# Kernel optimization log

Hardware: AMD Instinct MI355X
Metric: run time of the kernel (lower is better)

The kernel has to match this reference:

```python
import jax, jax.numpy as jnp
import numpy as np

B, T, S, D = 8, 512, 512, 1024
NUM_HEADS = 16
REUSE_HEADS = 8
NEW_HEADS = NUM_HEADS - REUSE_HEADS
KEY_DIM = 64
VALUE_DIM = 64
PE_MAX = 512  # pe_max_seq_length


def setup_inputs() -> dict:
    key = jax.random.key(0)
    ks = jax.random.split(key, 12)
    s = 0.02
    return {
        "query": jax.random.normal(ks[0], (B, T, D), jnp.float32),
        "value": jax.random.normal(ks[1], (B, S, D), jnp.float32),
        # scores reused from a previous layer (already softmaxed there)
        "reuse_attention_scores": jax.random.uniform(ks[2], (B, REUSE_HEADS, T, S), jnp.float32),
        "Wq": jax.random.normal(ks[3], (D, NEW_HEADS, KEY_DIM), jnp.float32) * s,
        "bq": jnp.zeros((NEW_HEADS, KEY_DIM), jnp.float32),
        "Wk": jax.random.normal(ks[4], (D, NEW_HEADS, KEY_DIM), jnp.float32) * s,
        "bk": jnp.zeros((NEW_HEADS, KEY_DIM), jnp.float32),
        "Wv": jax.random.normal(ks[5], (D, NUM_HEADS, VALUE_DIM), jnp.float32) * s,
        "bv": jnp.zeros((NUM_HEADS, VALUE_DIM), jnp.float32),
        # relative position embeddings: [1, new_heads, 2*PE_MAX - 1]
        "pos_emb": jax.random.truncated_normal(ks[6], -2.0, 2.0, (1, NEW_HEADS, 2 * PE_MAX - 1), jnp.float32) * 0.2,
        # output denses: one for reused heads (no bias), one for new heads (bias)
        "Wo_reuse": jax.random.normal(ks[7], (REUSE_HEADS, VALUE_DIM, D), jnp.float32) * s,
        "Wo_new": jax.random.normal(ks[8], (NEW_HEADS, VALUE_DIM, D), jnp.float32) * s,
        "bo": jnp.zeros((D,), jnp.float32),
    }


def reference(query, value, reuse_attention_scores, Wq, bq, Wk, bk, Wv, bv,
              pos_emb, Wo_reuse, Wo_new, bo):
    # projections (EinsumDense abc,cde->abde + bias over last two dims)
    q = jnp.einsum("btd,dnh->btnh", query, Wq) + bq           # [B,T,Hn,kd]
    k = jnp.einsum("bsd,dnh->bsnh", value, Wk) + bk           # [B,S,Hn,kd]
    v = jnp.einsum("bsd,dnh->bsnh", value, Wv) + bv           # [B,S,H,vd]
    v_reuse, v_new = v[:, :, :REUSE_HEADS, :], v[:, :, REUSE_HEADS:, :]

    # new-head scores: scaled QK^T  (dot_product_equation 'aecd,abcd->acbe')
    q = q * (1.0 / np.sqrt(float(KEY_DIM)))
    new_scores = jnp.einsum("bsnh,btnh->bnts", k, q)          # [B,Hn,T,S]

    # relative position bias: index = clip(key_pos - query_pos + PE_MAX-1)
    rel = jnp.arange(S)[None, :] - jnp.arange(T)[:, None] + (PE_MAX - 1)
    rel = jnp.clip(rel, 0, 2 * PE_MAX - 2)                    # [T,S]
    bias = pos_emb[0][:, rel]                                 # [Hn,T,S]
    new_scores = jax.nn.softmax(new_scores + bias[None], axis=-1)

    # reused heads consume previous-layer scores directly (dropout=0)
    reuse_scores = reuse_attention_scores[:, :REUSE_HEADS]
    out_reuse = jnp.einsum("bnts,bsnh->btnh", reuse_scores, v_reuse)
    out_new = jnp.einsum("bnts,bsnh->btnh", new_scores, v_new)

    # separate output projections, summed; bias only on the new-heads dense
    out = (jnp.einsum("btnh,nhd->btd", out_reuse, Wo_reuse)
           + jnp.einsum("btnh,nhd->btd", out_new, Wo_new) + bo)
    return out
```

## Files before the change

kernel.cpp:

```cpp
#include <hip/hip_runtime.h>
#include <hip/hip_bf16.h>

typedef __bf16 bf16_t;
typedef __bf16 bf16x8 __attribute__((ext_vector_type(8)));
typedef float  f32x4  __attribute__((ext_vector_type(4)));

#define GLDS(gsrc, ldst)                                                              \
  __builtin_amdgcn_global_load_lds(                                                   \
      (const __attribute__((address_space(1))) unsigned int*)(gsrc),                  \
      (__attribute__((address_space(3))) unsigned int*)(ldst), 16, 0, 0)

struct TArgs {
  const float* src[5];
  bf16_t* dst[5];
  int C[5], Ct[5], off[5], blk0[6];
  float scale[5];
};
struct CTArgs {
  const float* qa; bf16_t* qd;
  const float* va; bf16_t* vd;
  TArgs ta;
};
__global__ void k_convtrans(CTArgs ca) {
  __shared__ float tile[32][33];
  const int bid = blockIdx.x;
  if (bid < 4096) {
    int i = bid * 256 + threadIdx.x;
    const float* s; bf16_t* d;
    if (i < 524288) { s = ca.qa; d = ca.qd; } else { s = ca.va; d = ca.vd; i -= 524288; }
    const float4* p = reinterpret_cast<const float4*>(s) + 2 * (long)i;
    float4 x = p[0], y = p[1];
    bf16x8 o;
    o[0] = (bf16_t)x.x; o[1] = (bf16_t)x.y; o[2] = (bf16_t)x.z; o[3] = (bf16_t)x.w;
    o[4] = (bf16_t)y.x; o[5] = (bf16_t)y.y; o[6] = (bf16_t)y.z; o[7] = (bf16_t)y.w;
    reinterpret_cast<bf16x8*>(d)[i] = o;
    return;
  }
  const TArgs& ta = ca.ta;
  const int tb = bid - 4096;
  int s = 0;
  while (tb >= ta.blk0[s + 1]) ++s;
  const int bi = tb - ta.blk0[s];
  const int Ct = ta.Ct[s];
  const int c0 = (bi % Ct) * 32, r0 = (bi / Ct) * 32;
  const int C = ta.C[s];
  const float* src = ta.src[s];
  const int lx = threadIdx.x & 31, ly = threadIdx.x >> 5;
  #pragma unroll
  for (int i = 0; i < 32; i += 8)
    tile[ly + i][lx] = src[(long)(r0 + ly + i) * C + (c0 + lx)];
  __syncthreads();
  const float sc = ta.scale[s];
  bf16_t* dst = ta.dst[s];
  const int off = ta.off[s];
  #pragma unroll
  for (int i = 0; i < 32; i += 8)
    dst[(long)(c0 + ly + i) * 1024 + off + (r0 + lx)] = (bf16_t)(tile[lx][ly + i] * sc);
}

struct ProjItem {
  const bf16_t* A; const bf16_t* B; bf16_t* C; const float* bias;
  float bscale; int ldc; int writeT;
};
struct ProjArgs { ProjItem it[3]; };

__global__ __launch_bounds__(256)
void k_gemm_proj(ProjArgs pa) {
  __shared__ char smem[32768];
  const int bid = blockIdx.x;
  const int z = bid < 128 ? 0 : (bid < 256 ? 1 : 2);
  const int local = bid - (z == 0 ? 0 : (z == 1 ? 128 : 256));
  const ProjItem it = pa.it[z];
  const int t = threadIdx.x, lane = t & 63, wid = t >> 6;
  const int wr = wid >> 1, wc = wid & 1;
  const int m0 = (local & 31) * 128, n0 = (local >> 5) * 128;
  const int lhi = lane >> 4, llo = lane & 15;

  const bf16_t* Ab = it.A + (long)m0 * 1024;
  const bf16_t* Bb = it.B + (long)n0 * 1024;

  const int e0 = t * 8,        r0s = e0 >> 5, c0s = e0 & 31;
  const int e1 = (256 + t) * 8, r1s = e1 >> 5, c1s = e1 & 31;

#define PSTAGE(k0_, bsel)                                                     \
  { bf16_t* bA = (bf16_t*)(smem + (bsel) * 16384);                            \
    bf16_t* bB = (bf16_t*)(smem + (bsel) * 16384 + 8192);                     \
    GLDS(Ab + (long)r0s * 1024 + (k0_) + c0s, bA + wid * 512);                \
    GLDS(Ab + (long)r1s * 1024 + (k0_) + c1s, bA + 2048 + wid * 512);         \
    GLDS(Bb + (long)r0s * 1024 + (k0_) + c0s, bB + wid * 512);                \
    GLDS(Bb + (long)r1s * 1024 + (k0_) + c1s, bB + 2048 + wid * 512); }

  f32x4 acc[4][4] = {};
  PSTAGE(0, 0);
  __syncthreads();
  int cur = 0;
  for (int t32 = 0; t32 < 32; ++t32) {
    bf16_t* sA = (bf16_t*)(smem + cur * 16384);
    bf16_t* sB = (bf16_t*)(smem + cur * 16384 + 8192);
    bf16x8 a[4], b[4];
    #pragma unroll
    for (int mi = 0; mi < 4; ++mi)
      a[mi] = *reinterpret_cast<const bf16x8*>(sA + (wr * 64 + mi * 16 + llo) * 32 + lhi * 8);
    #pragma unroll
    for (int ni = 0; ni < 4; ++ni)
      b[ni] = *reinterpret_cast<const bf16x8*>(sB + (wc * 64 + ni * 16 + llo) * 32 + lhi * 8);
    if (t32 < 31) PSTAGE((t32 + 1) * 32, cur ^ 1);
    #pragma unroll
    for (int mi = 0; mi < 4; ++mi)
      #pragma unroll
      for (int ni = 0; ni < 4; ++ni)
        acc[mi][ni] = __builtin_amdgcn_mfma_f32_16x16x32_bf16(a[mi], b[ni], acc[mi][ni], 0, 0, 0);
    __syncthreads();
    cur ^= 1;
  }
#undef PSTAGE

  #pragma unroll
  for (int mi = 0; mi < 4; ++mi)
    #pragma unroll
    for (int ni = 0; ni < 4; ++ni) {
      const float bv = it.bias[n0 + wc * 64 + ni * 16 + llo] * it.bscale;
      #pragma unroll
      for (int r = 0; r < 4; ++r) acc[mi][ni][r] += bv;
    }

  if (!it.writeT) {
    bf16_t* E = (bf16_t*)smem;
    #pragma unroll
    for (int p = 0; p < 2; ++p) {
      if (wr == p) {
        #pragma unroll
        for (int mi = 0; mi < 4; ++mi)
          #pragma unroll
          for (int ni = 0; ni < 4; ++ni)
            #pragma unroll
            for (int r = 0; r < 4; ++r)
              E[(mi * 16 + lhi * 4 + r) * 136 + wc * 64 + ni * 16 + llo] = (bf16_t)acc[mi][ni][r];
      }
      __syncthreads();
      #pragma unroll
      for (int round = 0; round < 4; ++round) {
        const int row = (t >> 4) + round * 16;
        const int l16 = t & 15;
        float4 v = *reinterpret_cast<const float4*>((char*)E + row * 272 + l16 * 16);
        *reinterpret_cast<float4*>(it.C + (long)(m0 + p * 64 + row) * it.ldc + n0 + l16 * 8) = v;
      }
      __syncthreads();
    }
  } else {
    bf16_t* E = (bf16_t*)smem;
    #pragma unroll
    for (int p = 0; p < 2; ++p) {
      if (wr == p) {
        #pragma unroll
        for (int mi = 0; mi < 4; ++mi)
          #pragma unroll
          for (int ni = 0; ni < 4; ++ni)
            #pragma unroll
            for (int r = 0; r < 4; ++r)
              E[(wc * 64 + ni * 16 + llo) * 72 + mi * 16 + lhi * 4 + r] = (bf16_t)acc[mi][ni][r];
      }
      __syncthreads();
      #pragma unroll
      for (int round = 0; round < 4; ++round) {
        const int nr = (t >> 3) + round * 32;
        const int l8 = t & 7;
        float4 v = *reinterpret_cast<const float4*>((char*)E + nr * 144 + l8 * 16);
        *reinterpret_cast<float4*>(it.C + (long)(n0 + nr) * it.ldc + m0 + p * 64 + l8 * 8) = v;
      }
      __syncthreads();
    }
  }
}

__global__ __launch_bounds__(256)
void k_gemm_out(const bf16_t* __restrict__ A_, const bf16_t* __restrict__ B_,
                float* __restrict__ C_, const float* __restrict__ bias) {
  __shared__ char smem[24576];
  const int t = threadIdx.x, lane = t & 63, wid = t >> 6;
  const int wr = wid >> 1, wc = wid & 1;
  const int m0 = blockIdx.x * 64, n0 = blockIdx.y * 128;
  const int lhi = lane >> 4, llo = lane & 15;

  const bf16_t* Ab = A_ + (long)m0 * 1024;
  const bf16_t* Bb = B_ + (long)n0 * 1024;

  const int e0 = t * 8,        r0s = e0 >> 5, c0s = e0 & 31;
  const int e1 = (256 + t) * 8, r1s = e1 >> 5, c1s = e1 & 31;

#define OSTAGE(k0_, bsel)                                                     \
  { bf16_t* bA = (bf16_t*)(smem + (bsel) * 12288);                            \
    bf16_t* bB = (bf16_t*)(smem + (bsel) * 12288 + 4096);                     \
    GLDS(Ab + (long)r0s * 1024 + (k0_) + c0s, bA + wid * 512);                \
    GLDS(Bb + (long)r0s * 1024 + (k0_) + c0s, bB + wid * 512);                \
    GLDS(Bb + (long)r1s * 1024 + (k0_) + c1s, bB + 2048 + wid * 512); }

  f32x4 acc[2][4] = {};
  OSTAGE(0, 0);
  __syncthreads();
  int cur = 0;
  for (int t32 = 0; t32 < 32; ++t32) {
    bf16_t* sA = (bf16_t*)(smem + cur * 12288);
    bf16_t* sB = (bf16_t*)(smem + cur * 12288 + 4096);
    bf16x8 a[2], b[4];
    #pragma unroll
    for (int mi = 0; mi < 2; ++mi)
      a[mi] = *reinterpret_cast<const bf16x8*>(sA + (wr * 32 + mi * 16 + llo) * 32 + lhi * 8);
    #pragma unroll
    for (int ni = 0; ni < 4; ++ni)
      b[ni] = *reinterpret_cast<const bf16x8*>(sB + (wc * 64 + ni * 16 + llo) * 32 + lhi * 8);
    if (t32 < 31) OSTAGE((t32 + 1) * 32, cur ^ 1);
    #pragma unroll
    for (int mi = 0; mi < 2; ++mi)
      #pragma unroll
      for (int ni = 0; ni < 4; ++ni)
        acc[mi][ni] = __builtin_amdgcn_mfma_f32_16x16x32_bf16(a[mi], b[ni], acc[mi][ni], 0, 0, 0);
    __syncthreads();
    cur ^= 1;
  }
#undef OSTAGE

  #pragma unroll
  for (int mi = 0; mi < 2; ++mi)
    #pragma unroll
    for (int ni = 0; ni < 4; ++ni) {
      const float bv = bias[n0 + wc * 64 + ni * 16 + llo];
      #pragma unroll
      for (int r = 0; r < 4; ++r) acc[mi][ni][r] += bv;
    }

  float* E = (float*)smem;
  #pragma unroll
  for (int p = 0; p < 2; ++p) {
    if (wr == p) {
      #pragma unroll
      for (int mi = 0; mi < 2; ++mi)
        #pragma unroll
        for (int ni = 0; ni < 4; ++ni)
          #pragma unroll
          for (int r = 0; r < 4; ++r)
            E[(mi * 16 + lhi * 4 + r) * 132 + wc * 64 + ni * 16 + llo] = acc[mi][ni][r];
    }
    __syncthreads();
    #pragma unroll
    for (int round = 0; round < 4; ++round) {
      const int row = (t >> 5) + round * 8;
      const int l32 = t & 31;
      float4 v = *reinterpret_cast<const float4*>((char*)E + row * 528 + l32 * 16);
      *reinterpret_cast<float4*>(C_ + (long)(m0 + p * 32 + row) * 1024 + n0 + l32 * 4) = v;
    }
    __syncthreads();
  }
}

__global__ __launch_bounds__(256, 5)
void k_attn_all(const bf16_t* __restrict__ qb, const bf16_t* __restrict__ kb,
                const bf16_t* __restrict__ vbT, const float* __restrict__ pe,
                const float* __restrict__ reuse, bf16_t* __restrict__ om) {
  __shared__ char smem[28672];
  const int bid = blockIdx.x;
  const int r3 = bid % 3;
  const int q3 = bid / 3;
  const int lane = threadIdx.x & 63, w = threadIdx.x >> 6;
  const int lhi = lane >> 4, llo = lane & 15;

  if (r3 == 0) {
    float* pes = (float*)smem;
    char* KtB = smem + 4096;
    char* VtB = smem + 12288;
    char* PtB = smem + 20480 + w * 2048;

    const int fidx = q3;
    const int tt = fidx >> 6;
    const int bh = fidx & 63;
    const int b = bh >> 3, h = bh & 7;
    const int t0w = tt * 64 + w * 16;

    const bf16_t* Ksrc = kb + (long)(b * 512) * 512 + h * 64;
    const bf16_t* Vsrc = vbT + (long)(512 + h * 64) * 4096 + b * 512;
    const int krow = w * 16 + (lane >> 3);
    const int kcol = ((lane & 7) ^ (lane >> 3)) << 3;
    bf16_t* kdst = (bf16_t*)(KtB + w * 2048);
    bf16_t* vdst = (bf16_t*)(VtB + w * 2048);

#define STAGE_K(it_)                                                                   \
  { _Pragma("unroll")                                                                  \
    for (int g = 0; g < 2; ++g)                                                        \
      GLDS(Ksrc + (long)((it_) * 64 + krow + g * 8) * 512 + kcol, kdst + g * 512); }
#define STAGE_V(it_)                                                                   \
  { _Pragma("unroll")                                                                  \
    for (int g = 0; g < 2; ++g)                                                        \
      GLDS(Vsrc + (long)(krow + g * 8) * 4096 + (it_) * 64 + kcol, vdst + g * 512); }

    STAGE_K(0);
    STAGE_V(0);

    const bf16_t* Qb = qb + (long)(b * 512 + t0w + llo) * 512 + h * 64;
    bf16x8 qf0 = *reinterpret_cast<const bf16x8*>(Qb + lhi * 8);
    bf16x8 qf1 = *reinterpret_cast<const bf16x8*>(Qb + 32 + lhi * 8);
    for (int i = threadIdx.x; i < 1023; i += 256) pes[i] = pe[h * 1023 + i];

    f32x4 oacc[4] = {};
    float lr[4] = {0.f, 0.f, 0.f, 0.f};

    __syncthreads();

    for (int it = 0; it < 8; ++it) {
      const int s0 = it * 64;

      f32x4 acc[4] = {};
      #pragma unroll
      for (int st = 0; st < 4; ++st) {
        const int rowb = st * 16 + llo;
        const int sw = (rowb & 7) << 4;
        bf16x8 kf0 = *reinterpret_cast<const bf16x8*>(KtB + rowb * 128 + ((lhi * 16) ^ sw));
        bf16x8 kf1 = *reinterpret_cast<const bf16x8*>(KtB + rowb * 128 + ((64 + lhi * 16) ^ sw));
        acc[st] = __builtin_amdgcn_mfma_f32_16x16x32_bf16(qf0, kf0, acc[st], 0, 0, 0);
        acc[st] = __builtin_amdgcn_mfma_f32_16x16x32_bf16(qf1, kf1, acc[st], 0, 0, 0);
      }

      __syncthreads();
      if (it < 7) STAGE_K(it + 1);

      #pragma unroll
      for (int r = 0; r < 4; ++r) {
        const int tl = lhi * 4 + r;
        const int bidx = s0 + llo - (t0w + tl) + 511;
        const int swp = (tl & 7) << 4;
        float lp = 0.f;
        #pragma unroll
        for (int st = 0; st < 4; ++st) {
          const float e = __expf(acc[st][r] + pes[bidx + st * 16]);
          lp += e;
          *reinterpret_cast<bf16_t*>(PtB + tl * 128 + (((st * 16 + llo) * 2) ^ swp)) = (bf16_t)e;
        }
        lr[r] += lp;
      }

      const int swa = (llo & 7) << 4;
      #pragma unroll
      for (int ks = 0; ks < 2; ++ks) {
        bf16x8 pav = *reinterpret_cast<const bf16x8*>(PtB + llo * 128 + ((ks * 64 + lhi * 16) ^ swa));
        #pragma unroll
        for (int ni = 0; ni < 4; ++ni) {
          const int rowv = ni * 16 + llo;
          bf16x8 vf = *reinterpret_cast<const bf16x8*>(VtB + rowv * 128 + ((ks * 64 + lhi * 16) ^ ((rowv & 7) << 4)));
          oacc[ni] = __builtin_amdgcn_mfma_f32_16x16x32_bf16(pav, vf, oacc[ni], 0, 0, 0);
        }
      }

      __syncthreads();
      if (it < 7) STAGE_V(it + 1);
    }

    #pragma unroll
    for (int r = 0; r < 4; ++r) {
      lr[r] += __shfl_xor(lr[r], 1);
      lr[r] += __shfl_xor(lr[r], 2);
      lr[r] += __shfl_xor(lr[r], 4);
      lr[r] += __shfl_xor(lr[r], 8);
    }

    bf16_t* Ew = (bf16_t*)(smem + 4096 + w * 4096);
    #pragma unroll
    for (int ni = 0; ni < 4; ++ni)
      #pragma unroll
      for (int r = 0; r < 4; ++r)
        Ew[(lhi * 4 + r) * 72 + ni * 16 + llo] = (bf16_t)(oacc[ni][r] * (1.f / lr[r]));
    #pragma unroll
    for (int round = 0; round < 2; ++round) {
      const int lr8 = (lane >> 3) + round * 8;
      const int l8 = lane & 7;
      float4 v = *reinterpret_cast<const float4*>((char*)Ew + lr8 * 144 + l8 * 16);
      *reinterpret_cast<float4*>(om + (long)(b * 512 + t0w + lr8) * 1024 + 512 + h * 64 + l8 * 8) = v;
    }
#undef STAGE_K
#undef STAGE_V
    return;
  }

  typedef float RedRow[32][68];
  RedRow* red = (RedRow*)smem;
  const int pidx = q3 * 2 + (r3 - 1);
  const int bh = pidx & 63;
  const int mt = pidx >> 6;
  const int b = bh >> 3, head = bh & 7;
  const int m0 = mt * 32;
  const int ks0 = w * 128;

  const float*  Af = reuse + (long)b * 2097152 + (long)head * 262144;
  const bf16_t* Bp = vbT + (long)(head * 64) * 4096 + b * 512;

  f32x4 acc[2][4] = {};
  float4 Ax[2][2][2];
  bf16x8 Bx[2][4];

  #define PV_LOAD(kq, buf)                                                              \
    {                                                                                   \
      const int kk = ks0 + (kq) * 32 + lhi * 8;                                         \
      _Pragma("unroll")                                                                 \
      for (int mi = 0; mi < 2; ++mi) {                                                  \
        const float4* p = reinterpret_cast<const float4*>(Af + (long)(m0 + mi * 16 + llo) * 512 + kk); \
        Ax[buf][mi][0] = p[0];                                                          \
        Ax[buf][mi][1] = p[1];                                                          \
      }                                                                                 \
      _Pragma("unroll")                                                                 \
      for (int ni = 0; ni < 4; ++ni)                                                    \
        Bx[buf][ni] = *reinterpret_cast<const bf16x8*>(Bp + (long)(ni * 16 + llo) * 4096 + kk); \
    }

  PV_LOAD(0, 0);
  #pragma unroll
  for (int kq = 0; kq < 4; ++kq) {
    const int cb = kq & 1;
    if (kq < 3) {
      const int nb = (kq + 1) & 1;
      PV_LOAD(kq + 1, nb);
    }
    bf16x8 a[2];
    #pragma unroll
    for (int mi = 0; mi < 2; ++mi) {
      float4 x = Ax[cb][mi][0], y = Ax[cb][mi][1];
      bf16x8 tv;
      tv[0] = (bf16_t)x.x; tv[1] = (bf16_t)x.y; tv[2] = (bf16_t)x.z; tv[3] = (bf16_t)x.w;
      tv[4] = (bf16_t)y.x; tv[5] = (bf16_t)y.y; tv[6] = (bf16_t)y.z; tv[7] = (bf16_t)y.w;
      a[mi] = tv;
    }
    #pragma unroll
    for (int mi = 0; mi < 2; ++mi)
      #pragma unroll
      for (int ni = 0; ni < 4; ++ni)
        acc[mi][ni] = __builtin_amdgcn_mfma_f32_16x16x32_bf16(a[mi], Bx[cb][ni], acc[mi][ni], 0, 0, 0);
  }
  #undef PV_LOAD

  if (w >= 2) {
    #pragma unroll
    for (int mi = 0; mi < 2; ++mi)
      #pragma unroll
      for (int ni = 0; ni < 4; ++ni)
        #pragma unroll
        for (int r = 0; r < 4; ++r)
          red[w - 2][mi * 16 + lhi * 4 + r][ni * 16 + llo] = acc[mi][ni][r];
  }
  __syncthreads();
  if (w < 2) {
    #pragma unroll
    for (int mi = 0; mi < 2; ++mi)
      #pragma unroll
      for (int ni = 0; ni < 4; ++ni)
        #pragma unroll
        for (int r = 0; r < 4; ++r)
          acc[mi][ni][r] += red[w][mi * 16 + lhi * 4 + r][ni * 16 + llo];
  }
  __syncthreads();
  if (w == 1) {
    #pragma unroll
    for (int mi = 0; mi < 2; ++mi)
      #pragma unroll
      for (int ni = 0; ni < 4; ++ni)
        #pragma unroll
        for (int r = 0; r < 4; ++r)
          red[0][mi * 16 + lhi * 4 + r][ni * 16 + llo] = acc[mi][ni][r];
  }
  __syncthreads();
  if (w == 0) {
    bf16_t* E = (bf16_t*)&red[1][0][0];
    #pragma unroll
    for (int mi = 0; mi < 2; ++mi)
      #pragma unroll
      for (int ni = 0; ni < 4; ++ni)
        #pragma unroll
        for (int r = 0; r < 4; ++r) {
          const int mr = mi * 16 + lhi * 4 + r;
          const int nn = ni * 16 + llo;
          E[mr * 72 + nn] = (bf16_t)(acc[mi][ni][r] + red[0][mr][nn]);
        }
    bf16_t* Cb = om + (long)b * 524288 + head * 64;
    #pragma unroll
    for (int round = 0; round < 4; ++round) {
      const int row = (lane >> 3) + round * 8;
      const int l8 = lane & 7;
      float4 v = *reinterpret_cast<const float4*>((char*)E + row * 144 + l8 * 16);
      *reinterpret_cast<float4*>(Cb + (long)(m0 + row) * 1024 + l8 * 8) = v;
    }
  }
}

extern "C" void kernel_launch(void* const* d_in, const int* in_sizes, int n_in,
                              void* d_out, int out_size, void* d_ws, size_t ws_size,
                              hipStream_t stream) {
  const float* query = (const float*)d_in[0];
  const float* value = (const float*)d_in[1];
  const float* reuse = (const float*)d_in[2];
  const float* Wq    = (const float*)d_in[3];
  const float* bq    = (const float*)d_in[4];
  const float* Wk    = (const float*)d_in[5];
  const float* bk    = (const float*)d_in[6];
  const float* Wv    = (const float*)d_in[7];
  const float* bv    = (const float*)d_in[8];
  const float* pe    = (const float*)d_in[9];
  const float* WoR   = (const float*)d_in[10];
  const float* WoN   = (const float*)d_in[11];
  const float* bo    = (const float*)d_in[12];
  float* out = (float*)d_out;
  (void)in_sizes; (void)n_in; (void)out_size; (void)ws_size;

  char* w = (char*)d_ws;
  bf16_t* qx  = (bf16_t*)(w);
  bf16_t* vx  = (bf16_t*)(w + (8L  << 20));
  bf16_t* WqT = (bf16_t*)(w + (16L << 20));
  bf16_t* WkT = (bf16_t*)(w + (17L << 20));
  bf16_t* WvT = (bf16_t*)(w + (18L << 20));
  bf16_t* WoT = (bf16_t*)(w + (20L << 20));
  bf16_t* qb  = (bf16_t*)(w + (22L << 20));
  bf16_t* kb  = (bf16_t*)(w + (26L << 20));
  bf16_t* vbT = (bf16_t*)(w + (30L << 20));
  bf16_t* om  = (bf16_t*)(w + (38L << 20));

  CTArgs ca;
  ca.qa = query; ca.qd = qx; ca.va = value; ca.vd = vx;
  ca.ta.src[0] = Wq;  ca.ta.dst[0] = WqT; ca.ta.C[0] = 512;  ca.ta.Ct[0] = 16; ca.ta.off[0] = 0;   ca.ta.scale[0] = 0.125f;
  ca.ta.src[1] = Wk;  ca.ta.dst[1] = WkT; ca.ta.C[1] = 512;  ca.ta.Ct[1] = 16; ca.ta.off[1] = 0;   ca.ta.scale[1] = 1.f;
  ca.ta.src[2] = Wv;  ca.ta.dst[2] = WvT; ca.ta.C[2] = 1024; ca.ta.Ct[2] = 32; ca.ta.off[2] = 0;   ca.ta.scale[2] = 1.f;
  ca.ta.src[3] = WoR; ca.ta.dst[3] = WoT; ca.ta.C[3] = 1024; ca.ta.Ct[3] = 32; ca.ta.off[3] = 0;   ca.ta.scale[3] = 1.f;
  ca.ta.src[4] = WoN; ca.ta.dst[4] = WoT; ca.ta.C[4] = 1024; ca.ta.Ct[4] = 32; ca.ta.off[4] = 512; ca.ta.scale[4] = 1.f;
  ca.ta.blk0[0] = 0; ca.ta.blk0[1] = 512; ca.ta.blk0[2] = 1024; ca.ta.blk0[3] = 2048; ca.ta.blk0[4] = 2560; ca.ta.blk0[5] = 3072;
  k_convtrans<<<dim3(7168), 256, 0, stream>>>(ca);

  ProjArgs pa;
  pa.it[0] = { qx, WqT, qb,  bq, 0.125f, 512,  0 };
  pa.it[1] = { vx, WkT, kb,  bk, 1.f,    512,  0 };
  pa.it[2] = { vx, WvT, vbT, bv, 1.f,    4096, 1 };
  k_gemm_proj<<<dim3(512), 256, 0, stream>>>(pa);

  k_attn_all<<<dim3(1536), 256, 0, stream>>>(qb, kb, vbT, pe, reuse, om);

  k_gemm_out<<<dim3(64, 8), 256, 0, stream>>>(om, WoT, out, bo);
}
```

Baseline: 89.28 us.

## Double-buffer K/V tiles in LDS and deepen A prefetch in reuse path

In the new-head attention path, K and V tiles are now staged into two LDS buffers. The next iteration's tiles are issued at the top of each loop iteration, which removes one of the two per-iteration barriers. In the reuse-score path, loads of the fp32 score matrix are prefetched two steps ahead with a triple buffer, while V loads stay double-buffered. The cost is more LDS (45 KB vs 28 KB) and more registers, so launch bounds drop from 5 to 3 blocks per CU, which reduces occupancy.

```diff
diff --git a/kernel.cpp b/kernel.cpp
--- a/kernel.cpp
+++ b/kernel.cpp
@@ -253,11 +253,11 @@
   }
 }
 
-__global__ __launch_bounds__(256, 5)
+__global__ __launch_bounds__(256, 3)
 void k_attn_all(const bf16_t* __restrict__ qb, const bf16_t* __restrict__ kb,
                 const bf16_t* __restrict__ vbT, const float* __restrict__ pe,
                 const float* __restrict__ reuse, bf16_t* __restrict__ om) {
-  __shared__ char smem[28672];
+  __shared__ char smem[45056];
   const int bid = blockIdx.x;
   const int r3 = bid % 3;
   const int q3 = bid / 3;
@@ -266,9 +266,7 @@
 
   if (r3 == 0) {
     float* pes = (float*)smem;
-    char* KtB = smem + 4096;
-    char* VtB = smem + 12288;
-    char* PtB = smem + 20480 + w * 2048;
+    char* PtB = smem + 36864 + w * 2048;
 
     const int fidx = q3;
     const int tt = fidx >> 6;
@@ -280,20 +278,17 @@
     const bf16_t* Vsrc = vbT + (long)(512 + h * 64) * 4096 + b * 512;
     const int krow = w * 16 + (lane >> 3);
     const int kcol = ((lane & 7) ^ (lane >> 3)) << 3;
-    bf16_t* kdst = (bf16_t*)(KtB + w * 2048);
-    bf16_t* vdst = (bf16_t*)(VtB + w * 2048);
-
-#define STAGE_K(it_)                                                                   \
-  { _Pragma("unroll")                                                                  \
-    for (int g = 0; g < 2; ++g)                                                        \
-      GLDS(Ksrc + (long)((it_) * 64 + krow + g * 8) * 512 + kcol, kdst + g * 512); }
-#define STAGE_V(it_)                                                                   \
-  { _Pragma("unroll")                                                                  \
-    for (int g = 0; g < 2; ++g)                                                        \
-      GLDS(Vsrc + (long)(krow + g * 8) * 4096 + (it_) * 64 + kcol, vdst + g * 512); }
-
-    STAGE_K(0);
-    STAGE_V(0);
+
+#define STAGE_KV(it_, b_)                                                              \
+  { bf16_t* kdst = (bf16_t*)(smem + 4096 + (b_) * 8192 + w * 2048);                    \
+    bf16_t* vdst = (bf16_t*)(smem + 20480 + (b_) * 8192 + w * 2048);                   \
+    _Pragma("unroll")                                                                  \
+    for (int g = 0; g < 2; ++g) {                                                      \
+      GLDS(Ksrc + (long)((it_) * 64 + krow + g * 8) * 512 + kcol, kdst + g * 512);     \
+      GLDS(Vsrc + (long)(krow + g * 8) * 4096 + (it_) * 64 + kcol, vdst + g * 512);    \
+    } }
+
+    STAGE_KV(0, 0);
 
     const bf16_t* Qb = qb + (long)(b * 512 + t0w + llo) * 512 + h * 64;
     bf16x8 qf0 = *reinterpret_cast<const bf16x8*>(Qb + lhi * 8);
@@ -305,8 +300,13 @@
 
     __syncthreads();
 
+    int cur = 0;
     for (int it = 0; it < 8; ++it) {
       const int s0 = it * 64;
+      if (it < 7) STAGE_KV(it + 1, cur ^ 1);
+
+      const char* KtB = smem + 4096 + cur * 8192;
+      const char* VtB = smem + 20480 + cur * 8192;
 
       f32x4 acc[4] = {};
       #pragma unroll
@@ -319,9 +319,6 @@
         acc[st] = __builtin_amdgcn_mfma_f32_16x16x32_bf16(qf1, kf1, acc[st], 0, 0, 0);
       }
 
-      __syncthreads();
-      if (it < 7) STAGE_K(it + 1);
-
       #pragma unroll
       for (int r = 0; r < 4; ++r) {
         const int tl = lhi * 4 + r;
@@ -350,7 +347,7 @@
       }
 
       __syncthreads();
-      if (it < 7) STAGE_V(it + 1);
+      cur ^= 1;
     }
 
     #pragma unroll
@@ -374,8 +371,7 @@
       float4 v = *reinterpret_cast<const float4*>((char*)Ew + lr8 * 144 + l8 * 16);
       *reinterpret_cast<float4*>(om + (long)(b * 512 + t0w + lr8) * 1024 + 512 + h * 64 + l8 * 8) = v;
     }
-#undef STAGE_K
-#undef STAGE_V
+#undef STAGE_KV
     return;
   }
 
@@ -392,10 +388,10 @@
   const bf16_t* Bp = vbT + (long)(head * 64) * 4096 + b * 512;
 
   f32x4 acc[2][4] = {};
-  float4 Ax[2][2][2];
+  float4 Ax[3][2][2];
   bf16x8 Bx[2][4];
 
-  #define PV_LOAD(kq, buf)                                                              \
+  #define A_LOAD(kq, buf)                                                               \
     {                                                                                   \
       const int kk = ks0 + (kq) * 32 + lhi * 8;                                         \
       _Pragma("unroll")                                                                 \
@@ -404,23 +400,28 @@
         Ax[buf][mi][0] = p[0];                                                          \
         Ax[buf][mi][1] = p[1];                                                          \
       }                                                                                 \
+    }
+  #define B_LOAD(kq, buf)                                                               \
+    {                                                                                   \
+      const int kk = ks0 + (kq) * 32 + lhi * 8;                                         \
       _Pragma("unroll")                                                                 \
       for (int ni = 0; ni < 4; ++ni)                                                    \
         Bx[buf][ni] = *reinterpret_cast<const bf16x8*>(Bp + (long)(ni * 16 + llo) * 4096 + kk); \
     }
 
-  PV_LOAD(0, 0);
+  A_LOAD(0, 0);
+  A_LOAD(1, 1);
+  B_LOAD(0, 0);
   #pragma unroll
   for (int kq = 0; kq < 4; ++kq) {
-    const int cb = kq & 1;
-    if (kq < 3) {
-      const int nb = (kq + 1) & 1;
-      PV_LOAD(kq + 1, nb);
-    }
+    const int ca_ = kq % 3;
+    const int cb_ = kq & 1;
+    if (kq < 2) A_LOAD(kq + 2, (kq + 2) % 3);
+    if (kq < 3) B_LOAD(kq + 1, (kq + 1) & 1);
     bf16x8 a[2];
     #pragma unroll
     for (int mi = 0; mi < 2; ++mi) {
-      float4 x = Ax[cb][mi][0], y = Ax[cb][mi][1];
+      float4 x = Ax[ca_][mi][0], y = Ax[ca_][mi][1];
       bf16x8 tv;
       tv[0] = (bf16_t)x.x; tv[1] = (bf16_t)x.y; tv[2] = (bf16_t)x.z; tv[3] = (bf16_t)x.w;
       tv[4] = (bf16_t)y.x; tv[5] = (bf16_t)y.y; tv[6] = (bf16_t)y.z; tv[7] = (bf16_t)y.w;
@@ -430,9 +431,10 @@
     for (int mi = 0; mi < 2; ++mi)
       #pragma unroll
       for (int ni = 0; ni < 4; ++ni)
-        acc[mi][ni] = __builtin_amdgcn_mfma_f32_16x16x32_bf16(a[mi], Bx[cb][ni], acc[mi][ni], 0, 0, 0);
-  }
-  #undef PV_LOAD
+        acc[mi][ni] = __builtin_amdgcn_mfma_f32_16x16x32_bf16(a[mi], Bx[cb_][ni], acc[mi][ni], 0, 0, 0);
+  }
+  #undef A_LOAD
+  #undef B_LOAD
 
   if (w >= 2) {
     #pragma unroll
```

After: 91.49 us. 1.02x slower.
